# Optimization experiments

Hardware: AMD Instinct MI355X
Metric: run time of the kernel (lower is better)

The kernel has to match this reference:

```python
import jax, jax.numpy as jnp
import numpy as np

EPS = 1e-06

def _feature_map(x):
    # elu(x) + 1
    return jax.nn.elu(x) + 1.0

def setup_inputs() -> dict:
    key = jax.random.key(0)
    k1, k2, k3 = jax.random.split(key, 3)
    N, L, H, D = 4, 8192, 8, 128
    queries = jax.random.normal(k1, (N, L, H, D), dtype=jnp.float32)
    keys = jax.random.normal(k2, (N, L, H, D), dtype=jnp.float32)
    values = jax.random.normal(k3, (N, L, H, D), dtype=jnp.float32)
    threshold = jnp.array([0.1], dtype=jnp.float32)
    return {"queries": queries, "keys": keys, "values": values, "threshold": threshold}

def reference(queries, keys, values, threshold):
    Q = _feature_map(queries)            # [N,L,H,D]
    K = _feature_map(keys)               # [N,L,H,D]
    v_length = values.shape[1]
    v = values / v_length                # [N,L,H,V]
    KV = jnp.einsum('nshd,nshv->nhdv', K, v)            # [N,H,D,V]
    scores = jnp.einsum('nlhd,nhd->nlh', Q, K.sum(axis=1))  # [N,L,H]
    sparse = jnp.where(scores > threshold[0], scores, jnp.zeros_like(scores))
    Z = 1.0 / (sparse + EPS)             # [N,L,H]
    out = jnp.einsum('nlhd,nhdv,nlh->nlhv', Q, KV, Z) * v_length
    return out
```

## Files before the change

### kernel.cpp

```cpp
#include <hip/hip_runtime.h>
#include <stdint.h>


#define LSEQ 8192
#define NHD  1024
#define SP   20

typedef __attribute__((ext_vector_type(4))) float f32x4;
typedef __attribute__((ext_vector_type(8))) short bf16x8;
typedef unsigned short ushort_t;

static __device__ __forceinline__ unsigned short f2bf(float x) {
  union { float f; uint32_t u; } v; v.f = x;
  uint32_t r = v.u + 0x7FFFu + ((v.u >> 16) & 1u);
  return (unsigned short)(r >> 16);
}
static __device__ __forceinline__ uint32_t pack_bf(float a, float b) {
  return (uint32_t)f2bf(a) | ((uint32_t)f2bf(b) << 16);
}
static __device__ __forceinline__ float featmap(float x) {
  return x > 0.f ? x + 1.f : __expf(x);
}

#define BAR_LGKM() asm volatile("s_waitcnt lgkmcnt(0)\n\ts_barrier" ::: "memory")

__global__ __launch_bounds__(512, 4) void kv_direct(const float* __restrict__ keys,
                                                    const float* __restrict__ values,
                                                    ushort_t* __restrict__ kvpb,
                                                    float* __restrict__ kspart) {
  __shared__ uint32_t kls[128 * SP];
  __shared__ uint32_t vls[128 * SP];
  const int tid = threadIdx.x;
  const int chunk = blockIdx.x, CH = gridDim.x;
  const int h = blockIdx.y, n = blockIdx.z, nh = n * 8 + h;
  const int lane = tid & 63, w = tid >> 6;
  const int wr = w >> 2, wc = w & 3;
  const int lr = lane & 15, lg = lane >> 4;
  const int sPer = LSEQ / CH;
  const int steps = sPer / 32;

  const size_t gb = ((size_t)n * LSEQ + (size_t)chunk * sPer) * NHD + h * 128;
  const float* gk = keys + gb;
  const float* gv = values + gb;

  const int a = lane;
  const int fsw = 4 * ((a >> 2) & 3);
  const int wslot = (2 * w) ^ fsw;
  const int wbase0 = (2 * a) * SP + wslot;
  const int wbase1 = (2 * a + 1) * SP + wslot;

  f32x4 acc[4][2] = {};
  f32x4 ak[4] = {};
  bf16x8 ones;
  { uint32_t* u = (uint32_t*)&ones; u[0] = u[1] = u[2] = u[3] = 0x3F803F80u; }

#define ISSUE(T)                                                \
  do {                                                          \
    _Pragma("unroll") for (int j = 0; j < 4; ++j) {             \
      size_t off = (size_t)((T) * 32 + 4 * w + j) * NHD + 2 * a;\
      kr[j] = *(const float2*)(gk + off);                       \
      vr[j] = *(const float2*)(gv + off);                       \
    }                                                           \
  } while (0)

  float2 kr[4], vr[4];
  ISSUE(0);

  for (int t = 0; t < steps; ++t) {
    {
      uint2 kd0, kd1, vd0, vd1;
      kd0.x = pack_bf(featmap(kr[0].x), featmap(kr[1].x));
      kd0.y = pack_bf(featmap(kr[2].x), featmap(kr[3].x));
      kd1.x = pack_bf(featmap(kr[0].y), featmap(kr[1].y));
      kd1.y = pack_bf(featmap(kr[2].y), featmap(kr[3].y));
      vd0.x = pack_bf(vr[0].x, vr[1].x);
      vd0.y = pack_bf(vr[2].x, vr[3].x);
      vd1.x = pack_bf(vr[0].y, vr[1].y);
      vd1.y = pack_bf(vr[2].y, vr[3].y);
      *(uint2*)&kls[wbase0] = kd0;
      *(uint2*)&kls[wbase1] = kd1;
      *(uint2*)&vls[wbase0] = vd0;
      *(uint2*)&vls[wbase1] = vd1;
    }
    BAR_LGKM();
    if (t + 1 < steps) ISSUE(t + 1);
    {
      bf16x8 af[4], bfr[2];
#pragma unroll
      for (int fr = 0; fr < 4; ++fr) {
        int d = wr * 64 + fr * 16 + lr;
        af[fr] = *(const bf16x8*)&kls[d * SP + ((4 * lg) ^ (4 * ((d >> 3) & 3)))];
      }
#pragma unroll
      for (int fc = 0; fc < 2; ++fc) {
        int v = wc * 32 + fc * 16 + lr;
        bfr[fc] = *(const bf16x8*)&vls[v * SP + ((4 * lg) ^ (4 * ((v >> 3) & 3)))];
      }
#pragma unroll
      for (int fr = 0; fr < 4; ++fr)
#pragma unroll
        for (int fc = 0; fc < 2; ++fc)
          acc[fr][fc] = __builtin_amdgcn_mfma_f32_16x16x32_bf16(af[fr], bfr[fc], acc[fr][fc], 0, 0, 0);
      if (wc == 0) {
#pragma unroll
        for (int fr = 0; fr < 4; ++fr)
          ak[fr] = __builtin_amdgcn_mfma_f32_16x16x32_bf16(af[fr], ones, ak[fr], 0, 0, 0);
      }
    }
    BAR_LGKM();
  }
#undef ISSUE

  ushort_t* dst = kvpb + ((size_t)chunk * 32 + nh) * 16384;
#pragma unroll
  for (int fr = 0; fr < 4; ++fr)
#pragma unroll
    for (int fc = 0; fc < 2; ++fc) {
      int d0 = wr * 64 + fr * 16 + lg * 4;
      int v  = wc * 32 + fc * 16 + lr;
      *(uint2*)(dst + (size_t)v * 128 + d0) =
          make_uint2(pack_bf(acc[fr][fc][0], acc[fr][fc][1]),
                     pack_bf(acc[fr][fc][2], acc[fr][fc][3]));
    }
  if (wc == 0 && lr == 0) {
    float* ks = kspart + ((size_t)chunk * 32 + nh) * 128;
#pragma unroll
    for (int fr = 0; fr < 4; ++fr)
      *(float4*)(ks + wr * 64 + fr * 16 + lg * 4) =
          make_float4(ak[fr][0], ak[fr][1], ak[fr][2], ak[fr][3]);
  }
}

__global__ __launch_bounds__(256) void kv_merge(const ushort_t* __restrict__ kvpb,
                                                const float* __restrict__ kspart,
                                                ushort_t* __restrict__ kvb,
                                                float* __restrict__ ksumg,
                                                int CH) {
  const int nh = blockIdx.x, q = blockIdx.y, tid = threadIdx.x;
  const size_t off = (size_t)nh * 16384 + q * 4096;
#pragma unroll
  for (int i = 0; i < 4; ++i) {
    size_t idx = off + (size_t)(i * 256 + tid) * 4;
    f32x4 s = {};
    for (int c = 0; c < CH; ++c) {
      uint2 u = *(const uint2*)(kvpb + (size_t)c * 524288 + idx);
      s[0] += __uint_as_float(u.x << 16);
      s[1] += __uint_as_float(u.x & 0xFFFF0000u);
      s[2] += __uint_as_float(u.y << 16);
      s[3] += __uint_as_float(u.y & 0xFFFF0000u);
    }
    *(uint2*)(kvb + idx) = make_uint2(pack_bf(s[0], s[1]), pack_bf(s[2], s[3]));
  }
  if (q == 0 && tid < 128) {
    float s = 0.f;
    for (int c = 0; c < CH; ++c) s += kspart[((size_t)c * 32 + nh) * 128 + tid];
    ksumg[nh * 128 + tid] = s;
  }
}

__global__ __launch_bounds__(256, 4) void attn_out(const float* __restrict__ q,
                                                   const ushort_t* __restrict__ kvb,
                                                   const float* __restrict__ ksumg,
                                                   const float* __restrict__ thrp,
                                                   float* __restrict__ out) {
  __shared__ __align__(16) uint32_t As[128 * 17 * 4];
  __shared__ float zrow[128];

  const int tid = threadIdx.x;
  const int mc = blockIdx.x, nh = blockIdx.y;
  const int n = nh >> 3, h = nh & 7;
  const size_t qoff = ((size_t)(n * LSEQ + mc * 128)) * NHD + h * 128;
  const float thr = thrp[0];

  const int c4 = tid & 31;
  const float4 kk = *(const float4*)(ksumg + nh * 128 + c4 * 4);

#pragma unroll
  for (int it = 0; it < 16; ++it) {
    int rr = it * 8 + (tid >> 5);
    float4 qv = *(const float4*)(q + qoff + (size_t)rr * NHD + c4 * 4);
    float f0 = featmap(qv.x), f1 = featmap(qv.y), f2 = featmap(qv.z), f3 = featmap(qv.w);
    uint32_t* dst = &As[(rr * 17 + (c4 >> 1)) * 4 + (c4 & 1) * 2];
    dst[0] = pack_bf(f0, f1);
    dst[1] = pack_bf(f2, f3);
    float p = f0 * kk.x + f1 * kk.y + f2 * kk.z + f3 * kk.w;
    p += __shfl_xor(p, 1);  p += __shfl_xor(p, 2);  p += __shfl_xor(p, 4);
    p += __shfl_xor(p, 8);  p += __shfl_xor(p, 16);
    if (c4 == 0) {
      float sp = p > thr ? p : 0.f;
      zrow[rr] = 1.f / (sp + 1e-6f);
    }
  }
  __syncthreads();

  const int lane = tid & 63;
  const int w = tid >> 6;
  const int lr = lane & 15, lg = lane >> 4;
  const ushort_t* kvp = kvb + (size_t)nh * 16384;

  f32x4 acc0[8] = {};
  f32x4 acc1[8] = {};
#pragma unroll
  for (int ks = 0; ks < 4; ++ks) {
    const int c8 = ks * 4 + lg;
    const int dof = ks * 32 + lg * 8;
    const int r0 = w * 32 + lr;
    bf16x8 a0 = *(const bf16x8*)&As[(r0 * 17 + c8) * 4];
    bf16x8 a1 = *(const bf16x8*)&As[((r0 + 16) * 17 + c8) * 4];
#pragma unroll
    for (int ct = 0; ct < 8; ++ct) {
      bf16x8 bb = *(const bf16x8*)(kvp + (size_t)((ct * 16 + lr) * 128) + dof);
      acc0[ct] = __builtin_amdgcn_mfma_f32_16x16x32_bf16(a0, bb, acc0[ct], 0, 0, 0);
      acc1[ct] = __builtin_amdgcn_mfma_f32_16x16x32_bf16(a1, bb, acc1[ct], 0, 0, 0);
    }
  }

  float z0[4], z1[4];
#pragma unroll
  for (int j = 0; j < 4; ++j) {
    z0[j] = zrow[w * 32 + lg * 4 + j];
    z1[j] = zrow[w * 32 + 16 + lg * 4 + j];
  }
  float* op = out + qoff;
#pragma unroll
  for (int ct = 0; ct < 8; ++ct)
#pragma unroll
    for (int jj = 0; jj < 4; ++jj) {
      int row = w * 32 + lg * 4 + jj;
      op[(size_t)row * NHD + ct * 16 + lr]        = acc0[ct][jj] * z0[jj];
      op[(size_t)(row + 16) * NHD + ct * 16 + lr] = acc1[ct][jj] * z1[jj];
    }
}

extern "C" void kernel_launch(void* const* d_in, const int* in_sizes, int n_in,
                              void* d_out, int out_size, void* d_ws, size_t ws_size,
                              hipStream_t stream) {
  const float* queries   = (const float*)d_in[0];
  const float* keys      = (const float*)d_in[1];
  const float* values    = (const float*)d_in[2];
  const float* threshold = (const float*)d_in[3];
  float* out = (float*)d_out;

  int CH = 32;
  while (CH > 1 &&
         (size_t)CH * (524288 * 2 + 32 * 128 * 4) + (size_t)32 * 16384 * 2 + 32 * 128 * 4 > ws_size)
    CH >>= 1;
  ushort_t* kvpb = (ushort_t*)d_ws;
  float* kspart  = (float*)(kvpb + (size_t)CH * 524288);
  ushort_t* kvb  = (ushort_t*)(kspart + (size_t)CH * 32 * 128);
  float* ksumg   = (float*)(kvb + (size_t)32 * 16384);

  kv_direct<<<dim3(CH, 8, 4), 512, 0, stream>>>(keys, values, kvpb, kspart);
  kv_merge<<<dim3(32, 4), 256, 0, stream>>>(kvpb, kspart, kvb, ksumg, CH);
  attn_out<<<dim3(64, 32), 256, 0, stream>>>(queries, kvb, ksumg, threshold, out);
}
```

Baseline: 200.3 us.

## Restructure KV accumulation kernel into 128-row burst tiles with 4-wave blocks

Replaces the 512-thread kv_direct kernel with a 256-thread kv_burst kernel. Each block now loads 128 sequence rows per tile using float4 global loads held in registers, instead of 32 rows per step with float2 loads. Cross-half-wave shuffles transpose the packed bf16 data into a wider, swizzled LDS layout, so each barrier pair covers four MFMA k-steps and each wave computes a 64x64 output tile. The goal is fewer barriers, more bytes in flight per load and better MFMA operand reuse, at the cost of much higher register pressure (32 float4 staging registers plus 16 accumulators), larger LDS and lower occupancy.

Result: slower. 225.0 us (+12.3%).

```diff
diff --git a/kernel.cpp b/kernel.cpp
--- a/kernel.cpp
+++ b/kernel.cpp
@@ -4,7 +4,7 @@
 
 #define LSEQ 8192
 #define NHD  1024
-#define SP   20
+#define SPN  68
 
 typedef __attribute__((ext_vector_type(4))) float f32x4;
 typedef __attribute__((ext_vector_type(8))) short bf16x8;
@@ -24,82 +24,100 @@
 
 #define BAR_LGKM() asm volatile("s_waitcnt lgkmcnt(0)\n\ts_barrier" ::: "memory")
 
-__global__ __launch_bounds__(512, 4) void kv_direct(const float* __restrict__ keys,
-                                                    const float* __restrict__ values,
-                                                    ushort_t* __restrict__ kvpb,
-                                                    float* __restrict__ kspart) {
-  __shared__ uint32_t kls[128 * SP];
-  __shared__ uint32_t vls[128 * SP];
+__global__ __launch_bounds__(256, 2) void kv_burst(const float* __restrict__ keys,
+                                                   const float* __restrict__ values,
+                                                   ushort_t* __restrict__ kvpb,
+                                                   float* __restrict__ kspart) {
+  __shared__ uint32_t kls[128 * SPN];
+  __shared__ uint32_t vls[128 * SPN];
   const int tid = threadIdx.x;
   const int chunk = blockIdx.x, CH = gridDim.x;
   const int h = blockIdx.y, n = blockIdx.z, nh = n * 8 + h;
   const int lane = tid & 63, w = tid >> 6;
-  const int wr = w >> 2, wc = w & 3;
+  const int wr = w >> 1, wc = w & 1;
   const int lr = lane & 15, lg = lane >> 4;
   const int sPer = LSEQ / CH;
-  const int steps = sPer / 32;
+  const int tiles = sPer / 128;
 
   const size_t gb = ((size_t)n * LSEQ + (size_t)chunk * sPer) * NHD + h * 128;
   const float* gk = keys + gb;
   const float* gv = values + gb;
 
-  const int a = lane;
-  const int fsw = 4 * ((a >> 2) & 3);
-  const int wslot = (2 * w) ^ fsw;
-  const int wbase0 = (2 * a) * SP + wslot;
-  const int wbase1 = (2 * a + 1) * SP + wslot;
-
-  f32x4 acc[4][2] = {};
+  const int av = lane >> 5;
+  const int q  = lane & 31;
+  const int swzq = 4 * ((q >> 1) & 3);
+
+  f32x4 acc[4][4] = {};
   f32x4 ak[4] = {};
   bf16x8 ones;
   { uint32_t* u = (uint32_t*)&ones; u[0] = u[1] = u[2] = u[3] = 0x3F803F80u; }
 
-#define ISSUE(T)                                                \
-  do {                                                          \
-    _Pragma("unroll") for (int j = 0; j < 4; ++j) {             \
-      size_t off = (size_t)((T) * 32 + 4 * w + j) * NHD + 2 * a;\
-      kr[j] = *(const float2*)(gk + off);                       \
-      vr[j] = *(const float2*)(gv + off);                       \
-    }                                                           \
+  float4 kr4[16], vr4[16];
+
+#define ISSUE(TB)                                                          \
+  do {                                                                     \
+    _Pragma("unroll") for (int sub = 0; sub < 8; ++sub)                    \
+      _Pragma("unroll") for (int i = 0; i < 2; ++i) {                      \
+        size_t off = (size_t)((TB) * 128 + 32 * w + 4 * sub + av + 2 * i) * NHD + 4 * q; \
+        kr4[sub * 2 + i] = *(const float4*)(gk + off);                     \
+        vr4[sub * 2 + i] = *(const float4*)(gv + off);                     \
+      }                                                                    \
   } while (0)
 
-  float2 kr[4], vr[4];
+#define STAGE()                                                            \
+  do {                                                                     \
+    _Pragma("unroll") for (int sub = 0; sub < 8; ++sub) {                  \
+      const int base0 = (4 * q) * SPN + ((16 * w + 2 * sub + av) ^ swzq);  \
+      uint2 u0, u1, p0, p1, lo, hi;                                        \
+      u0.x = pack_bf(featmap(kr4[2 * sub].x), featmap(kr4[2 * sub].y));    \
+      u0.y = pack_bf(featmap(kr4[2 * sub].z), featmap(kr4[2 * sub].w));    \
+      u1.x = pack_bf(featmap(kr4[2 * sub + 1].x), featmap(kr4[2 * sub + 1].y)); \
+      u1.y = pack_bf(featmap(kr4[2 * sub + 1].z), featmap(kr4[2 * sub + 1].w)); \
+      p0.x = __shfl_xor((int)u0.x, 32); p0.y = __shfl_xor((int)u0.y, 32);  \
+      p1.x = __shfl_xor((int)u1.x, 32); p1.y = __shfl_xor((int)u1.y, 32);  \
+      lo.x = av ? p1.x : u0.x;  lo.y = av ? p1.y : u0.y;                   \
+      hi.x = av ? u1.x : p0.x;  hi.y = av ? u1.y : p0.y;                   \
+      kls[base0]           = (lo.x & 0xFFFFu) | (hi.x << 16);              \
+      kls[base0 + SPN]     = (lo.x >> 16) | (hi.x & 0xFFFF0000u);          \
+      kls[base0 + 2 * SPN] = (lo.y & 0xFFFFu) | (hi.y << 16);              \
+      kls[base0 + 3 * SPN] = (lo.y >> 16) | (hi.y & 0xFFFF0000u);          \
+      u0.x = pack_bf(vr4[2 * sub].x, vr4[2 * sub].y);                      \
+      u0.y = pack_bf(vr4[2 * sub].z, vr4[2 * sub].w);                      \
+      u1.x = pack_bf(vr4[2 * sub + 1].x, vr4[2 * sub + 1].y);              \
+      u1.y = pack_bf(vr4[2 * sub + 1].z, vr4[2 * sub + 1].w);              \
+      p0.x = __shfl_xor((int)u0.x, 32); p0.y = __shfl_xor((int)u0.y, 32);  \
+      p1.x = __shfl_xor((int)u1.x, 32); p1.y = __shfl_xor((int)u1.y, 32);  \
+      lo.x = av ? p1.x : u0.x;  lo.y = av ? p1.y : u0.y;                   \
+      hi.x = av ? u1.x : p0.x;  hi.y = av ? u1.y : p0.y;                   \
+      vls[base0]           = (lo.x & 0xFFFFu) | (hi.x << 16);              \
+      vls[base0 + SPN]     = (lo.x >> 16) | (hi.x & 0xFFFF0000u);          \
+      vls[base0 + 2 * SPN] = (lo.y & 0xFFFFu) | (hi.y << 16);              \
+      vls[base0 + 3 * SPN] = (lo.y >> 16) | (hi.y & 0xFFFF0000u);          \
+    }                                                                      \
+  } while (0)
+
   ISSUE(0);
-
-  for (int t = 0; t < steps; ++t) {
-    {
-      uint2 kd0, kd1, vd0, vd1;
-      kd0.x = pack_bf(featmap(kr[0].x), featmap(kr[1].x));
-      kd0.y = pack_bf(featmap(kr[2].x), featmap(kr[3].x));
-      kd1.x = pack_bf(featmap(kr[0].y), featmap(kr[1].y));
-      kd1.y = pack_bf(featmap(kr[2].y), featmap(kr[3].y));
-      vd0.x = pack_bf(vr[0].x, vr[1].x);
-      vd0.y = pack_bf(vr[2].x, vr[3].x);
-      vd1.x = pack_bf(vr[0].y, vr[1].y);
-      vd1.y = pack_bf(vr[2].y, vr[3].y);
-      *(uint2*)&kls[wbase0] = kd0;
-      *(uint2*)&kls[wbase1] = kd1;
-      *(uint2*)&vls[wbase0] = vd0;
-      *(uint2*)&vls[wbase1] = vd1;
-    }
+  for (int tb = 0; tb < tiles; ++tb) {
+    STAGE();
     BAR_LGKM();
-    if (t + 1 < steps) ISSUE(t + 1);
-    {
-      bf16x8 af[4], bfr[2];
+    if (tb + 1 < tiles) ISSUE(tb + 1);
+#pragma unroll
+    for (int ks = 0; ks < 4; ++ks) {
+      bf16x8 af[4], bfr[4];
 #pragma unroll
       for (int fr = 0; fr < 4; ++fr) {
         int d = wr * 64 + fr * 16 + lr;
-        af[fr] = *(const bf16x8*)&kls[d * SP + ((4 * lg) ^ (4 * ((d >> 3) & 3)))];
+        af[fr] = *(const bf16x8*)&kls[d * SPN + ((16 * ks + 4 * lg) ^ (4 * ((d >> 3) & 3)))];
       }
 #pragma unroll
-      for (int fc = 0; fc < 2; ++fc) {
-        int v = wc * 32 + fc * 16 + lr;
-        bfr[fc] = *(const bf16x8*)&vls[v * SP + ((4 * lg) ^ (4 * ((v >> 3) & 3)))];
+      for (int fc = 0; fc < 4; ++fc) {
+        int v = wc * 64 + fc * 16 + lr;
+        bfr[fc] = *(const bf16x8*)&vls[v * SPN + ((16 * ks + 4 * lg) ^ (4 * ((v >> 3) & 3)))];
       }
 #pragma unroll
       for (int fr = 0; fr < 4; ++fr)
 #pragma unroll
-        for (int fc = 0; fc < 2; ++fc)
+        for (int fc = 0; fc < 4; ++fc)
           acc[fr][fc] = __builtin_amdgcn_mfma_f32_16x16x32_bf16(af[fr], bfr[fc], acc[fr][fc], 0, 0, 0);
       if (wc == 0) {
 #pragma unroll
@@ -110,14 +128,15 @@
     BAR_LGKM();
   }
 #undef ISSUE
+#undef STAGE
 
   ushort_t* dst = kvpb + ((size_t)chunk * 32 + nh) * 16384;
 #pragma unroll
   for (int fr = 0; fr < 4; ++fr)
 #pragma unroll
-    for (int fc = 0; fc < 2; ++fc) {
+    for (int fc = 0; fc < 4; ++fc) {
       int d0 = wr * 64 + fr * 16 + lg * 4;
-      int v  = wc * 32 + fc * 16 + lr;
+      int v  = wc * 64 + fc * 16 + lr;
       *(uint2*)(dst + (size_t)v * 128 + d0) =
           make_uint2(pack_bf(acc[fr][fc][0], acc[fr][fc][1]),
                      pack_bf(acc[fr][fc][2], acc[fr][fc][3]));
@@ -242,7 +261,7 @@
   float* out = (float*)d_out;
 
   int CH = 32;
-  while (CH > 1 &&
+  while (CH > 2 &&
          (size_t)CH * (524288 * 2 + 32 * 128 * 4) + (size_t)32 * 16384 * 2 + 32 * 128 * 4 > ws_size)
     CH >>= 1;
   ushort_t* kvpb = (ushort_t*)d_ws;
@@ -250,7 +269,7 @@
   ushort_t* kvb  = (ushort_t*)(kspart + (size_t)CH * 32 * 128);
   float* ksumg   = (float*)(kvb + (size_t)32 * 16384);
 
-  kv_direct<<<dim3(CH, 8, 4), 512, 0, stream>>>(keys, values, kvpb, kspart);
+  kv_burst<<<dim3(CH, 8, 4), 256, 0, stream>>>(keys, values, kvpb, kspart);
   kv_merge<<<dim3(32, 4), 256, 0, stream>>>(kvpb, kspart, kvb, ksumg, CH);
   attn_out<<<dim3(64, 32), 256, 0, stream>>>(queries, kvb, ksumg, threshold, out);
 }
```
